# Kernel optimization log

Measured on AMD Instinct MI355X. Metric: run time of the kernel, lower is better.

## Reference

```python
import jax, jax.numpy as jnp
import numpy as np

SQRT2 = 1.4142135623730951
INV_SQRT_2PI = 0.3989422804014327

def Phi(x):
    # standard normal CDF
    return 0.5 * (1.0 + jax.lax.erf(x / SQRT2))

def phi(x):
    # standard normal pdf
    return INV_SQRT_2PI * jnp.exp(-0.5 * x * x)

def phip(x):
    # derivative of the standard normal pdf
    return -x * phi(x)


def setup_inputs() -> dict:
    key = jax.random.key(0)
    k1, k2, k3 = jax.random.split(key, 3)
    bs, n, c, d = 4, 256, 96, 2
    xin = jax.random.normal(k1, (bs, n, d), dtype=jnp.float32)
    meanin = jax.random.normal(k2, (bs, n, c), dtype=jnp.float32)
    # SPD spatial covariance: A A^T / n + 0.5 I (eigenvalues >> 1e-6)
    A = jax.random.normal(k3, (bs, n, n), dtype=jnp.float32)
    kin = A @ jnp.swapaxes(A, -1, -2) / n + 0.5 * jnp.eye(n, dtype=jnp.float32)
    return {"xin": xin, "meanin": meanin, "kin": kin}


def reference(xin, meanin, kin):
    bs, n, c = meanin.shape
    eye = jnp.eye(n, dtype=kin.dtype)
    kin = kin + eye * 1e-6
    kdiag = jnp.diagonal(kin, axis1=-2, axis2=-1)            # (bs,n)
    stdin = jnp.sqrt(jnp.clip(kdiag[..., None], 1e-8))       # (bs,n,1)
    z = meanin / stdin
    Phis = Phi(z)
    phis = phi(z)
    Eh = meanin * Phis + stdin * phis                        # (bs,n,c)

    # 2x2 matrix K12 per (i,j): [[k_ii, k_ij], [k_ji, k_jj]] -- kept as scalars
    m00 = kdiag[:, :, None]                                  # (bs,n,1) -> broadcast (bs,n,n)
    m11 = kdiag[:, None, :]
    m01 = kin
    m10 = jnp.swapaxes(kin, -1, -2)

    # matrix square root of 2x2 SPD: (M + sqrt(det) I) / sqrt(tr + 2 sqrt(det))
    det = m00 * m11 - m01 * m10
    tr = m00 + m11
    s = jnp.sqrt(jnp.clip(det, 1e-8))
    t = jnp.clip(jnp.sqrt(tr + 2.0 * s), 1e-8)
    s00 = (m00 + s) / t
    s01 = m01 / t
    s10 = m10 / t
    s11 = (m11 + s) / t

    # inverse of the 2x2 sqrt
    dS = jnp.clip(s00 * s11 - s01 * s10, 1e-8)
    i00 = s11 / dS
    i01 = -s01 / dS
    i10 = -s10 / dS
    i11 = s00 / dS

    mi = meanin[:, :, None, :]                               # (bs,n,1,c)
    mj = meanin[:, None, :, :]                               # (bs,1,n,c)

    u1 = i00[..., None] * mi + i01[..., None] * mj           # (bs,n,n,c)
    u2 = i10[..., None] * mi + i11[..., None] * mj
    Phi1 = Phi(u1)
    Phi2 = Phi(u2)
    p1 = phi(u1)
    p2 = phi(u2)

    Psi = Phi1 * Phi2
    psi1 = p1 * Phi2
    psi2 = Phi1 * p2

    EhhT_Psi = (mi * mj + kin[..., None]) * Psi
    EhhT_psi1 = (mj * s00[..., None] + mi * s10[..., None]) * psi1
    EhhT_psi2 = (mj * s01[..., None] + mi * s11[..., None]) * psi2

    SHPhiS11 = s00[..., None] * s01[..., None] * phip(u1) * Phi2
    SHPhiS12 = s01[..., None] * s01[..., None] * p1 * p2
    SHPhiS22 = s01[..., None] * s11[..., None] * Phi1 * phip(u2)
    SHPhiS = SHPhiS11 + 2.0 * SHPhiS12 + SHPhiS22

    EhhT = EhhT_Psi + (EhhT_psi1 + EhhT_psi2) + SHPhiS
    covar = (EhhT - Eh[:, :, None, :] * Eh[:, None, :, :]).mean(-1)   # (bs,n,n)

    dvals = jnp.clip(
        ((meanin ** 2 + stdin ** 2) * Phis + meanin * stdin * phis - Eh ** 2).mean(-1),
        1e-6,
    )                                                        # (bs,n)
    diag_covar = dvals[..., None] * eye                      # diag_embed
    full_covar = jnp.where(diag_covar > 1e-7, diag_covar, covar)
    return (xin, Eh, full_covar + eye * 1e-6)
```

## Files before the change

### kernel.cpp

```cpp
#include <hip/hip_runtime.h>
#include <math.h>

#define BSZ 4
#define NN  256
#define CC  96
#define TT  16
#define NTILES 136
#define RSTR 100
#define ARR  (TT * RSTR)

#define XIN_OFF  0
#define EH_OFF   2048
#define COV_OFF  100352

#define INV_SQRT_2PI 0.3989422804014327f
#define EXP2C       -0.7213475204444817f
#define PHI_P   0.33267253f
#define PHI_C1  0.1740121f
#define PHI_C2 -0.0479399f
#define PHI_C3  0.3739278f

__device__ __forceinline__ float phi_from_exp_s(float u, float e) {
    float t  = __builtin_amdgcn_rcpf(__builtin_fmaf(PHI_P, fabsf(u), 1.0f));
    float hp = __builtin_fmaf(__builtin_fmaf(PHI_C3, t, PHI_C2), t, PHI_C1) * t * e;
    return 0.5f + __builtin_copysignf(0.5f - hp, u);
}

__device__ __forceinline__ int tri_offset(int k) {
    return k * TT - (k * (k - 1)) / 2;
}
__device__ __forceinline__ void tri_decode(int t, int& ti, int& tj) {
    float disc = 1089.0f - 8.0f * (float)t;
    ti = (int)((33.0f - __builtin_amdgcn_sqrtf(disc)) * 0.5f);
    while (tri_offset(ti + 1) <= t) ++ti;
    while (tri_offset(ti) > t) --ti;
    tj = ti + (t - tri_offset(ti));
}

__global__ __launch_bounds__(512) void relu_cov_fused(
    const float* __restrict__ xin, const float* __restrict__ meanin,
    const float* __restrict__ kin, float* __restrict__ out)
{
    const int blk = blockIdx.x;
    const int b   = blk / NTILES;
    const int t   = blk - b * NTILES;
    const int tid = threadIdx.x;

    int ti, tj;
    tri_decode(t, ti, tj);
    const bool diag = (ti == tj);

    __shared__ __align__(16) float lds[4 * ARR];
    __shared__ float red[512];
    __shared__ float srowS[32], srowR[32], srowV[32];
    float* const smi = lds;
    float* const sEi = lds + ARR;
    float* const smj = lds + 2 * ARR;
    float* const sEj = lds + 3 * ARR;

    if (tid < 32) {
        int row = (tid < 16) ? (ti * TT + tid) : (tj * TT + (tid - 16));
        float kd  = kin[((size_t)(b * NN + row)) * NN + row] + 1e-6f;
        float var = fmaxf(kd, 1e-8f);
        float st  = __builtin_amdgcn_sqrtf(var);
        srowV[tid] = var;
        srowS[tid] = st;
        srowR[tid] = __builtin_amdgcn_rcpf(st);
    }
#pragma unroll
    for (int it = 0; it < 2; ++it) {
        int k = tid + it * 512;
        if (k < 768) {
            int arr = k / 384;
            int rem = k - arr * 384;
            int r   = rem / 24;
            int q   = rem - r * 24;
            int row = ((arr == 0) ? ti : tj) * TT + r;
            float4 v = *((const float4*)(meanin + ((size_t)(b * NN + row)) * CC) + q);
            *(float4*)(lds + arr * 2 * ARR + r * RSTR + q * 4) = v;
        }
    }
    __syncthreads();

#pragma unroll
    for (int it = 0; it < 6; ++it) {
        int k   = tid + it * 512;
        int arr = k / 1536;
        int rem = k - arr * 1536;
        int r   = rem / 96;
        int c   = rem - r * 96;
        float m  = lds[arr * 2 * ARR + r * RSTR + c];
        float st = srowS[arr * 16 + r];
        float rs = srowR[arr * 16 + r];
        float z  = m * rs;
        float e  = __builtin_amdgcn_exp2f(z * z * EXP2C);
        float Ph = phi_from_exp_s(z, e);
        float Eh = __builtin_fmaf(m, Ph, st * (INV_SQRT_2PI * e));
        lds[(arr * 2 + 1) * ARR + r * RSTR + c] = Eh;
    }
    __syncthreads();

    if (diag) {
#pragma unroll
        for (int it = 0; it < 3; ++it) {
            int k = tid + it * 512;
            int r = k / 96, c = k - r * 96;
            out[EH_OFF + ((size_t)(b * NN + ti * TT + r)) * CC + c] = sEi[r * RSTR + c];
        }
        if (tid < 32) {
            int r = tid >> 1, d = tid & 1;
            size_t o = ((size_t)(b * NN + ti * TT + r)) * 2 + d;
            out[XIN_OFF + o] = xin[o];
        }
        {
            int r = tid >> 5, s = tid & 31;
            float st = srowS[r], var = srowV[r], rs = srowR[r];
            float dsum = 0.0f;
#pragma unroll
            for (int dc = 0; dc < 3; ++dc) {
                int c = s * 3 + dc;
                float m  = smi[r * RSTR + c];
                float Eh = sEi[r * RSTR + c];
                float z  = m * rs;
                float e  = __builtin_amdgcn_exp2f(z * z * EXP2C);
                float Ph = phi_from_exp_s(z, e);
                float ph = INV_SQRT_2PI * e;
                float dt = __builtin_fmaf(__builtin_fmaf(m, m, var), Ph,
                           __builtin_fmaf(m * st, ph, -Eh * Eh));
                dsum += dt;
            }
            dsum += __shfl_down(dsum, 16, 32);
            dsum += __shfl_down(dsum,  8, 32);
            dsum += __shfl_down(dsum,  4, 32);
            dsum += __shfl_down(dsum,  2, 32);
            dsum += __shfl_down(dsum,  1, 32);
            if (s == 0) {
                float dval = fmaxf(dsum * (1.0f / 96.0f), 1e-6f);
                int row = ti * TT + r;
                out[COV_OFF + ((size_t)(b * NN + row)) * NN + row] = dval + 1e-6f;
            }
        }
    }

    const int p     = tid & 255;
    const int h     = tid >> 8;
    const int i_loc = p >> 4;
    const int j_loc = p & 15;
    const int i = ti * TT + i_loc;
    const int j = tj * TT + j_loc;

    const float m00 = srowV[i_loc];
    const float m11 = srowV[16 + j_loc];
    const float m01 = kin[((size_t)(b * NN + i)) * NN + j];

    const float det = __builtin_fmaf(-m01, m01, m00 * m11);
    const float s   = __builtin_amdgcn_sqrtf(fmaxf(det, 1e-8f));
    const float tt  = fmaxf(__builtin_amdgcn_sqrtf(m00 + m11 + 2.0f * s), 1e-8f);
    const float rt  = __builtin_amdgcn_rcpf(tt);
    const float s00 = (m00 + s) * rt;
    const float s01 = m01 * rt;
    const float s11 = (m11 + s) * rt;
    const float dS  = fmaxf(__builtin_fmaf(-s01, s01, s00 * s11), 1e-8f);
    const float rdS = __builtin_amdgcn_rcpf(dS);
    const float i00 = s11 * rdS;
    const float i01 = -s01 * rdS;
    const float i11 = s00 * rdS;
    const float qd = -INV_SQRT_2PI * s01 * s01 * s01 * rdS;
    const float qj =  INV_SQRT_2PI * s00 * s00 * s11 * rdS;
    const float qi =  INV_SQRT_2PI * s00 * s11 * s11 * rdS;
    const float c2 = 2.0f * INV_SQRT_2PI * INV_SQRT_2PI * s01 * s01;

    const float* Lmi = smi + i_loc * RSTR + h * 48;
    const float* LEi = sEi + i_loc * RSTR + h * 48;
    const float* Lmj = smj + j_loc * RSTR + h * 48;
    const float* LEj = sEj + j_loc * RSTR + h * 48;

    float acc0 = 0.0f, acc1 = 0.0f, acc2 = 0.0f, acc3 = 0.0f;

    auto elem = [&](float mi, float mjv, float Ei, float Ej, float& acc) {
        float u1 = __builtin_fmaf(i01, mjv, i00 * mi);
        float u2 = __builtin_fmaf(i11, mjv, i01 * mi);
        float e1 = __builtin_amdgcn_exp2f(u1 * u1 * EXP2C);
        float e2 = __builtin_amdgcn_exp2f(u2 * u2 * EXP2C);
        float d1 = __builtin_fmaf(PHI_P, fabsf(u1), 1.0f);
        float d2 = __builtin_fmaf(PHI_P, fabsf(u2), 1.0f);
        float rp = __builtin_amdgcn_rcpf(d1 * d2);
        float t1 = d2 * rp;
        float t2 = d1 * rp;
        float hp1 = __builtin_fmaf(__builtin_fmaf(PHI_C3, t1, PHI_C2), t1, PHI_C1) * t1 * e1;
        float hp2 = __builtin_fmaf(__builtin_fmaf(PHI_C3, t2, PHI_C2), t2, PHI_C1) * t2 * e2;
        float Phi1 = 0.5f + __builtin_copysignf(0.5f - hp1, u1);
        float Phi2 = 0.5f + __builtin_copysignf(0.5f - hp2, u2);
        float a  = __builtin_fmaf(mi, mjv, m01);
        float bb = __builtin_fmaf(qd, mi, qj * mjv);
        float cc = __builtin_fmaf(qi, mi, qd * mjv);
        float ta = __builtin_fmaf(a,  Phi1, bb * e1);
        float tb = __builtin_fmaf(cc, Phi1, c2 * e1);
        acc = __builtin_fmaf(Phi2, ta, acc);
        acc = __builtin_fmaf(e2,   tb, acc);
        acc = __builtin_fmaf(-Ei,  Ej, acc);
    };

#pragma unroll 4
    for (int q = 0; q < 12; ++q) {
        float4 mi4 = *(const float4*)(Lmi + q * 4);
        float4 mj4 = *(const float4*)(Lmj + q * 4);
        float4 Ei4 = *(const float4*)(LEi + q * 4);
        float4 Ej4 = *(const float4*)(LEj + q * 4);
        elem(mi4.x, mj4.x, Ei4.x, Ej4.x, acc0);
        elem(mi4.y, mj4.y, Ei4.y, Ej4.y, acc1);
        elem(mi4.z, mj4.z, Ei4.z, Ej4.z, acc2);
        elem(mi4.w, mj4.w, Ei4.w, Ej4.w, acc3);
    }

    red[tid] = (acc0 + acc1) + (acc2 + acc3);
    __syncthreads();

    if (tid < 256 && i < j) {
        float v = (red[tid] + red[tid + 256]) * (1.0f / 96.0f);
        out[COV_OFF + ((size_t)(b * NN + i)) * NN + j] = v;
        out[COV_OFF + ((size_t)(b * NN + j)) * NN + i] = v;
    }
}

extern "C" void kernel_launch(void* const* d_in, const int* in_sizes, int n_in,
                              void* d_out, int out_size, void* d_ws, size_t ws_size,
                              hipStream_t stream) {
    const float* xin    = (const float*)d_in[0];
    const float* meanin = (const float*)d_in[1];
    const float* kin    = (const float*)d_in[2];
    float* out = (float*)d_out;

    relu_cov_fused<<<BSZ * NTILES, 512, 0, stream>>>(xin, meanin, kin, out);
}
```

Baseline: 77.19 us.

## Register-block 2x2 output pairs per thread and split channels into eight groups

Each thread now computes a 2x2 block of (i,j) covariance entries over 12 channels, instead of one entry over 48 channels. This reuses each LDS float4 load across two pairs and cuts shared-memory read traffic per element. In exchange, every thread recomputes the 2x2 sqrt/inverse coefficients for four pairs, holds many more live registers, and the final reduction sums eight partials per entry.

```diff
diff --git a/kernel.cpp b/kernel.cpp
--- a/kernel.cpp
+++ b/kernel.cpp
@@ -51,7 +51,7 @@
     const bool diag = (ti == tj);
 
     __shared__ __align__(16) float lds[4 * ARR];
-    __shared__ float red[512];
+    __shared__ float red[8 * 256];
     __shared__ float srowS[32], srowR[32], srowV[32];
     float* const smi = lds;
     float* const sEi = lds + ARR;
@@ -142,44 +142,51 @@
         }
     }
 
-    const int p     = tid & 255;
-    const int h     = tid >> 8;
-    const int i_loc = p >> 4;
-    const int j_loc = p & 15;
-    const int i = ti * TT + i_loc;
-    const int j = tj * TT + j_loc;
-
-    const float m00 = srowV[i_loc];
-    const float m11 = srowV[16 + j_loc];
-    const float m01 = kin[((size_t)(b * NN + i)) * NN + j];
-
-    const float det = __builtin_fmaf(-m01, m01, m00 * m11);
-    const float s   = __builtin_amdgcn_sqrtf(fmaxf(det, 1e-8f));
-    const float tt  = fmaxf(__builtin_amdgcn_sqrtf(m00 + m11 + 2.0f * s), 1e-8f);
-    const float rt  = __builtin_amdgcn_rcpf(tt);
-    const float s00 = (m00 + s) * rt;
-    const float s01 = m01 * rt;
-    const float s11 = (m11 + s) * rt;
-    const float dS  = fmaxf(__builtin_fmaf(-s01, s01, s00 * s11), 1e-8f);
-    const float rdS = __builtin_amdgcn_rcpf(dS);
-    const float i00 = s11 * rdS;
-    const float i01 = -s01 * rdS;
-    const float i11 = s00 * rdS;
-    const float qd = -INV_SQRT_2PI * s01 * s01 * s01 * rdS;
-    const float qj =  INV_SQRT_2PI * s00 * s00 * s11 * rdS;
-    const float qi =  INV_SQRT_2PI * s00 * s11 * s11 * rdS;
-    const float c2 = 2.0f * INV_SQRT_2PI * INV_SQRT_2PI * s01 * s01;
-
-    const float* Lmi = smi + i_loc * RSTR + h * 48;
-    const float* LEi = sEi + i_loc * RSTR + h * 48;
-    const float* Lmj = smj + j_loc * RSTR + h * 48;
-    const float* LEj = sEj + j_loc * RSTR + h * 48;
-
-    float acc0 = 0.0f, acc1 = 0.0f, acc2 = 0.0f, acc3 = 0.0f;
-
-    auto elem = [&](float mi, float mjv, float Ei, float Ej, float& acc) {
-        float u1 = __builtin_fmaf(i01, mjv, i00 * mi);
-        float u2 = __builtin_fmaf(i11, mjv, i01 * mi);
+    const int pt = tid & 63;
+    const int ch = tid >> 6;
+    const int ia = (pt >> 3) * 2;
+    const int jb = (pt & 7) * 2;
+    const int c0 = ch * 12;
+
+    float Ci00[2][2], Ci01[2][2], Ci11[2][2], Cm01[2][2];
+    float Cqd[2][2], Cqj[2][2], Cqi[2][2], Cc2[2][2];
+    {
+        const float* kb = kin + (size_t)b * NN * NN;
+#pragma unroll
+        for (int ii = 0; ii < 2; ++ii) {
+            const int gi = ti * TT + ia + ii;
+            const float m00 = srowV[ia + ii];
+            float2 k2 = *(const float2*)(kb + (size_t)gi * NN + tj * TT + jb);
+#pragma unroll
+            for (int jj = 0; jj < 2; ++jj) {
+                const float m11 = srowV[16 + jb + jj];
+                const float m01 = (jj == 0) ? k2.x : k2.y;
+                const float det = __builtin_fmaf(-m01, m01, m00 * m11);
+                const float s   = __builtin_amdgcn_sqrtf(fmaxf(det, 1e-8f));
+                const float tt  = fmaxf(__builtin_amdgcn_sqrtf(m00 + m11 + 2.0f * s), 1e-8f);
+                const float rt  = __builtin_amdgcn_rcpf(tt);
+                const float s00 = (m00 + s) * rt;
+                const float s01 = m01 * rt;
+                const float s11 = (m11 + s) * rt;
+                const float dS  = fmaxf(__builtin_fmaf(-s01, s01, s00 * s11), 1e-8f);
+                const float rdS = __builtin_amdgcn_rcpf(dS);
+                Ci00[ii][jj] = s11 * rdS;
+                Ci01[ii][jj] = -s01 * rdS;
+                Ci11[ii][jj] = s00 * rdS;
+                Cm01[ii][jj] = m01;
+                Cqd[ii][jj]  = -INV_SQRT_2PI * s01 * s01 * s01 * rdS;
+                Cqj[ii][jj]  =  INV_SQRT_2PI * s00 * s00 * s11 * rdS;
+                Cqi[ii][jj]  =  INV_SQRT_2PI * s00 * s11 * s11 * rdS;
+                Cc2[ii][jj]  = 2.0f * INV_SQRT_2PI * INV_SQRT_2PI * s01 * s01;
+            }
+        }
+    }
+
+    float acc[2][2] = {{0.0f, 0.0f}, {0.0f, 0.0f}};
+
+    auto elem = [&](int ii, int jj, float mi, float mjv, float Ei, float Ej) {
+        float u1 = __builtin_fmaf(Ci01[ii][jj], mjv, Ci00[ii][jj] * mi);
+        float u2 = __builtin_fmaf(Ci11[ii][jj], mjv, Ci01[ii][jj] * mi);
         float e1 = __builtin_amdgcn_exp2f(u1 * u1 * EXP2C);
         float e2 = __builtin_amdgcn_exp2f(u2 * u2 * EXP2C);
         float d1 = __builtin_fmaf(PHI_P, fabsf(u1), 1.0f);
@@ -191,35 +198,58 @@
         float hp2 = __builtin_fmaf(__builtin_fmaf(PHI_C3, t2, PHI_C2), t2, PHI_C1) * t2 * e2;
         float Phi1 = 0.5f + __builtin_copysignf(0.5f - hp1, u1);
         float Phi2 = 0.5f + __builtin_copysignf(0.5f - hp2, u2);
-        float a  = __builtin_fmaf(mi, mjv, m01);
-        float bb = __builtin_fmaf(qd, mi, qj * mjv);
-        float cc = __builtin_fmaf(qi, mi, qd * mjv);
+        float a  = __builtin_fmaf(mi, mjv, Cm01[ii][jj]);
+        float bb = __builtin_fmaf(Cqd[ii][jj], mi, Cqj[ii][jj] * mjv);
+        float cc = __builtin_fmaf(Cqi[ii][jj], mi, Cqd[ii][jj] * mjv);
         float ta = __builtin_fmaf(a,  Phi1, bb * e1);
-        float tb = __builtin_fmaf(cc, Phi1, c2 * e1);
-        acc = __builtin_fmaf(Phi2, ta, acc);
-        acc = __builtin_fmaf(e2,   tb, acc);
-        acc = __builtin_fmaf(-Ei,  Ej, acc);
+        float tb = __builtin_fmaf(cc, Phi1, Cc2[ii][jj] * e1);
+        float& A = acc[ii][jj];
+        A = __builtin_fmaf(Phi2, ta, A);
+        A = __builtin_fmaf(e2,   tb, A);
+        A = __builtin_fmaf(-Ei,  Ej, A);
     };
 
-#pragma unroll 4
-    for (int q = 0; q < 12; ++q) {
-        float4 mi4 = *(const float4*)(Lmi + q * 4);
-        float4 mj4 = *(const float4*)(Lmj + q * 4);
-        float4 Ei4 = *(const float4*)(LEi + q * 4);
-        float4 Ej4 = *(const float4*)(LEj + q * 4);
-        elem(mi4.x, mj4.x, Ei4.x, Ej4.x, acc0);
-        elem(mi4.y, mj4.y, Ei4.y, Ej4.y, acc1);
-        elem(mi4.z, mj4.z, Ei4.z, Ej4.z, acc2);
-        elem(mi4.w, mj4.w, Ei4.w, Ej4.w, acc3);
-    }
-
-    red[tid] = (acc0 + acc1) + (acc2 + acc3);
+#pragma unroll
+    for (int q = 0; q < 3; ++q) {
+        const int co = c0 + q * 4;
+        float4 mi4[2], Ei4[2], mj4[2], Ej4[2];
+#pragma unroll
+        for (int r = 0; r < 2; ++r) {
+            mi4[r] = *(const float4*)(smi + (ia + r) * RSTR + co);
+            Ei4[r] = *(const float4*)(sEi + (ia + r) * RSTR + co);
+            mj4[r] = *(const float4*)(smj + (jb + r) * RSTR + co);
+            Ej4[r] = *(const float4*)(sEj + (jb + r) * RSTR + co);
+        }
+#pragma unroll
+        for (int ii = 0; ii < 2; ++ii) {
+#pragma unroll
+            for (int jj = 0; jj < 2; ++jj) {
+                elem(ii, jj, mi4[ii].x, mj4[jj].x, Ei4[ii].x, Ej4[jj].x);
+                elem(ii, jj, mi4[ii].y, mj4[jj].y, Ei4[ii].y, Ej4[jj].y);
+                elem(ii, jj, mi4[ii].z, mj4[jj].z, Ei4[ii].z, Ej4[jj].z);
+                elem(ii, jj, mi4[ii].w, mj4[jj].w, Ei4[ii].w, Ej4[jj].w);
+            }
+        }
+    }
+
+#pragma unroll
+    for (int ii = 0; ii < 2; ++ii)
+#pragma unroll
+        for (int jj = 0; jj < 2; ++jj)
+            red[ch * 256 + (ia + ii) * 16 + (jb + jj)] = acc[ii][jj];
     __syncthreads();
 
-    if (tid < 256 && i < j) {
-        float v = (red[tid] + red[tid + 256]) * (1.0f / 96.0f);
-        out[COV_OFF + ((size_t)(b * NN + i)) * NN + j] = v;
-        out[COV_OFF + ((size_t)(b * NN + j)) * NN + i] = v;
+    if (tid < 256) {
+        float sum = 0.0f;
+#pragma unroll
+        for (int k = 0; k < 8; ++k) sum += red[k * 256 + tid];
+        const int i = ti * TT + (tid >> 4);
+        const int j = tj * TT + (tid & 15);
+        if (i < j) {
+            float v = sum * (1.0f / 96.0f);
+            out[COV_OFF + ((size_t)(b * NN + i)) * NN + j] = v;
+            out[COV_OFF + ((size_t)(b * NN + j)) * NN + i] = v;
+        }
     }
 }
 
```

Result: no change. 76.90 us (-0.4%).
